# Kernel tuning notes

Hardware: AMD Instinct MI355X
Metric: run time of the kernel (lower is better)

## Reference

```python
import jax, jax.numpy as jnp
import numpy as np

B, C, H, W = 16, 256, 64, 64
E = 8           # num_experts
TOPK = 2
HID = int(C * 2.0)  # hidden_mult = 2.0 -> 512


def setup_inputs() -> dict:
    key = jax.random.key(0)
    ks = jax.random.split(key, 6)
    x = jax.random.normal(ks[0], (B, C, H, W), dtype=jnp.float32)
    Wr = jax.random.normal(ks[1], (C, E), dtype=jnp.float32) * 0.02
    br = jnp.zeros((E,), dtype=jnp.float32)
    W1 = jax.random.normal(ks[2], (E, C, HID), dtype=jnp.float32) * 0.02
    b1 = jnp.zeros((E, HID), dtype=jnp.float32)
    W2 = jax.random.normal(ks[3], (E, HID, C), dtype=jnp.float32) * 0.02
    b2 = jnp.zeros((E, C), dtype=jnp.float32)
    # nn.Parameter(torch.zeros(1)) in the original; use a small random value so
    scale = jax.random.normal(ks[4], (1,), dtype=jnp.float32) * 0.1
    return {"x": x, "Wr": Wr, "br": br, "W1": W1, "b1": b1,
            "W2": W2, "b2": b2, "scale": scale}


def reference(x, Wr, br, W1, b1, W2, b2, scale):
    b, c, h, w = x.shape
    tokens = jnp.transpose(x, (0, 2, 3, 1)).reshape(b, h * w, c)  # (B, T, C)
    logits = tokens @ Wr + br                                      # (B, T, E)
    topv, topi = jax.lax.top_k(logits, TOPK)                       # (B, T, K)
    wts = jax.nn.softmax(topv, axis=-1)                            # (B, T, K)

    out = jnp.zeros_like(tokens)
    num_experts = Wr.shape[1]
    for e in range(num_experts):
        # combine weight for expert e: sum of routing weights where selected
        we = jnp.sum(jnp.where(topi == e, wts, 0.0), axis=-1)      # (B, T)
        hdn = jax.nn.gelu(tokens @ W1[e] + b1[e], approximate=False)
        y = hdn @ W2[e] + b2[e]                                    # (B, T, C)
        out = out + y * we[..., None]

    out = jnp.transpose(out.reshape(b, h, w, c), (0, 3, 1, 2))     # (B, C, H, W)
    return x + scale[0] * out
```

## Files before the change

### kernel.cpp

```cpp
#include <hip/hip_runtime.h>
#include <hip/hip_bf16.h>
#include <math.h>

#define HW   4096
#define CCH  256
#define NE   8
#define HID  512
#define NTOK 65536
#define PADH 260

typedef short s16x8 __attribute__((ext_vector_type(8)));
typedef float f32x4 __attribute__((ext_vector_type(4)));
typedef unsigned short u16x8 __attribute__((ext_vector_type(8)));
typedef unsigned short u16x4 __attribute__((ext_vector_type(4)));

__device__ __forceinline__ float fast_gelu(float v) {
    float v2 = v * v;
    float s  = v * fmaf(0.10294324f, v2, 2.3022079f);
    float e  = exp2f(-s);
    return v * __builtin_amdgcn_rcpf(1.0f + e);
}

__device__ __forceinline__ float bfbits2f(unsigned short h) {
    return __uint_as_float(((unsigned)h) << 16);
}

__device__ __forceinline__ short f2bf_bits(float f) {
    __hip_bfloat16 b = __float2bfloat16(f);
    return *reinterpret_cast<short*>(&b);
}

__device__ __forceinline__ unsigned short f2bf_ubits(float f) {
    __hip_bfloat16 b = __float2bfloat16(f);
    return *reinterpret_cast<unsigned short*>(&b);
}

__global__ __launch_bounds__(256) void k_transpose_both(
    const float* __restrict__ W1, const float* __restrict__ W2,
    __hip_bfloat16* __restrict__ w1t, __hip_bfloat16* __restrict__ w2t,
    int* __restrict__ meta)
{
    __shared__ float t[64][65];
    if (blockIdx.x == 0 && threadIdx.x < 16) meta[threadIdx.x] = 0;
    int bb = blockIdx.x;
    const float* in; __hip_bfloat16* out; int R, CC;
    if (bb < 256) { in = W1; out = w1t; R = 256; CC = 512; }
    else          { in = W2; out = w2t; R = 512; CC = 256; bb -= 256; }
    int tilesC = CC >> 6;
    int per = (R >> 6) * tilesC;
    int e = bb / per, tt = bb % per;
    int r0 = (tt / tilesC) << 6, c0 = (tt % tilesC) << 6;
    const float* ip = in + (size_t)e * R * CC;
    __hip_bfloat16* op = out + (size_t)e * R * CC;
    int lane = threadIdx.x & 63, g = threadIdx.x >> 6;
    for (int i = 0; i < 16; i++) {
        int r = i * 4 + g;
        t[r][lane] = ip[(size_t)(r0 + r) * CC + c0 + lane];
    }
    __syncthreads();
    for (int i = 0; i < 16; i++) {
        int r = i * 4 + g;
        op[(size_t)(c0 + r) * R + r0 + lane] = __float2bfloat16(t[lane][r]);
    }
}

__global__ __launch_bounds__(256) void k_router(
    const float* __restrict__ x, const float* __restrict__ Wr, const float* __restrict__ br,
    __hip_bfloat16* __restrict__ tokens, int* __restrict__ pair, float2* __restrict__ wts,
    int* __restrict__ meta )
{
    __shared__ float xt[CCH][33];
    __shared__ float wrp[2304];
    __shared__ float lg[32][NE];
    __shared__ int lc[NE];
    int tid = threadIdx.x;
    int n0 = blockIdx.x * 32;
    int b = n0 >> 12, p0 = n0 & 4095;
    const float* xb = x + (size_t)b * CCH * HW + p0;
    for (int i = tid; i < CCH * NE; i += 256) wrp[i] = Wr[i];
    if (tid < NE) lc[tid] = 0;
    __syncthreads();
    int j = tid & 31, cg = tid >> 5;
    float pacc[8];
#pragma unroll
    for (int e = 0; e < 8; e++) pacc[e] = 0.f;
    for (int i = 0; i < 32; i++) {
        int c = cg + 8 * i;
        float xv = xb[(size_t)c * HW + j];
        xt[c][j] = xv;
        const float4* wp = (const float4*)(wrp + c * 8);
        float4 wa = wp[0], wb2 = wp[1];
        pacc[0] = fmaf(xv, wa.x, pacc[0]);
        pacc[1] = fmaf(xv, wa.y, pacc[1]);
        pacc[2] = fmaf(xv, wa.z, pacc[2]);
        pacc[3] = fmaf(xv, wa.w, pacc[3]);
        pacc[4] = fmaf(xv, wb2.x, pacc[4]);
        pacc[5] = fmaf(xv, wb2.y, pacc[5]);
        pacc[6] = fmaf(xv, wb2.z, pacc[6]);
        pacc[7] = fmaf(xv, wb2.w, pacc[7]);
    }
    __syncthreads();
    float* plg = wrp;
#pragma unroll
    for (int e = 0; e < 8; e++) plg[(cg * 32 + j) * 9 + e] = pacc[e];
    __syncthreads();
    {
        int jj = tid & 31, e = tid >> 5;
        float s = br[e];
#pragma unroll
        for (int g = 0; g < 8; g++) s += plg[(g * 32 + jj) * 9 + e];
        lg[jj][e] = s;
    }
    __syncthreads();
    if (tid < 32) {
        float v0 = -1e30f, v1 = -1e30f; int i0 = 0, i1 = 0;
        for (int e = 0; e < NE; e++) {
            float l = lg[tid][e];
            if (l > v0)      { v1 = v0; i1 = i0; v0 = l; i0 = e; }
            else if (l > v1) { v1 = l; i1 = e; }
        }
        float e1 = expf(v1 - v0);
        float s = 1.0f + e1;
        wts[n0 + tid] = make_float2(1.0f / s, e1 / s);
        pair[n0 + tid] = i0 | (i1 << 8);
        atomicAdd(&lc[i0], 1);
        atomicAdd(&lc[i1], 1);
    }
    __syncthreads();
    if (tid < NE && lc[tid] > 0) atomicAdd(&meta[tid], lc[tid]);
#pragma unroll
    for (int i = 0; i < 4; i++) {
        int c0 = (cg + 8 * i) * 8;
        s16x8 v;
#pragma unroll
        for (int k = 0; k < 8; k++) v[k] = f2bf_bits(xt[c0 + k][j]);
        *(s16x8*)(tokens + (size_t)(n0 + j) * CCH + c0) = v;
    }
}

__global__ __launch_bounds__(256) void k_scatter(
    const int* __restrict__ pair, const float2* __restrict__ wts,
    int* __restrict__ meta, int* __restrict__ assign_tok, float* __restrict__ assign_w,
    int2* __restrict__ tok_slots)
{
    __shared__ int lcount[NE];
    __shared__ int lbase[NE];
    __shared__ int soff[NE];
    int tid = threadIdx.x;
    int n = blockIdx.x * 256 + tid;
    if (tid < NE) lcount[tid] = 0;
    __syncthreads();
    int pr = pair[n];
    int e0 = pr & 0xff, e1 = (pr >> 8) & 0xff;
    int p0 = atomicAdd(&lcount[e0], 1);
    int p1 = atomicAdd(&lcount[e1], 1);
    __syncthreads();
    if (tid == 0) {
        int off = 0, toff = 0;
        for (int ee = 0; ee < NE; ee++) {
            soff[ee] = off;
            int c = meta[ee];
            if (blockIdx.x == 0) { meta[16 + ee] = off; meta[25 + ee] = toff; }
            off += c;
            toff += (c + 63) >> 6;
        }
        if (blockIdx.x == 0) { meta[24] = off; meta[33] = toff; meta[34] = toff; }
    }
    if (tid < NE) lbase[tid] = atomicAdd(&meta[8 + tid], lcount[tid]);
    __syncthreads();
    float2 w = wts[n];
    int s0 = soff[e0] + lbase[e0] + p0;
    int s1 = soff[e1] + lbase[e1] + p1;
    assign_tok[s0] = n; assign_w[s0] = w.x;
    assign_tok[s1] = n; assign_w[s1] = w.y;
    tok_slots[n] = make_int2(s0, s1);
}

__global__ __launch_bounds__(512, 4) void k_expert(
    const __hip_bfloat16* __restrict__ tokens,
    const __hip_bfloat16* __restrict__ w1t,
    const __hip_bfloat16* __restrict__ w2t,
    const float* __restrict__ b1, const float* __restrict__ b2,
    const int* __restrict__ meta,
    const int* __restrict__ assign_tok, const float* __restrict__ assign_w,
    __hip_bfloat16* __restrict__ ybuf)
{
    __shared__ __align__(16) __hip_bfloat16 Af[64 * 256];
    __shared__ __align__(16) __hip_bfloat16 Hs[64 * PADH];
    __shared__ float wrow[64];
    __shared__ int trow[64];

    int total = meta[34];
    int swz = (int)blockIdx.x;
    int bid = (swz & 7) * 257 + (swz >> 3);
    if (bid >= total) return;
    int e = 0;
    while (e < 7 && bid >= meta[25 + e + 1]) e++;
    int tile = bid - meta[25 + e];
    int cnt = meta[e];
    int r0 = tile << 6;
    int abase = meta[16 + e] + r0;
    int nrows = cnt - r0; if (nrows > 64) nrows = 64;

    int tid = threadIdx.x;
    if (tid < 64) {
        if (tid < nrows) { trow[tid] = assign_tok[abase + tid]; wrow[tid] = assign_w[abase + tid]; }
        else             { trow[tid] = 0; wrow[tid] = 0.0f; }
    }
    __syncthreads();

    {
        uint4* dst = (uint4*)Af;
#pragma unroll
        for (int j = 0; j < 4; j++) {
            int row = j * 16 + (tid & 15);
            int chunk = (tid >> 4) & 31;
            dst[j * 512 + tid] = ((const uint4*)(tokens + (size_t)trow[row] * CCH))[chunk];
        }
    }

    int lane = tid & 63, wv = tid >> 6;
    int quad = lane >> 4, l15 = lane & 15;

    const __hip_bfloat16* w1e = w1t + (size_t)e * HID * CCH;
    const __hip_bfloat16* w2e = w2t + (size_t)e * CCH * HID;
    const float* b1e = b1 + e * HID;
    const float* b2e = b2 + e * CCH;

    const s16x8* apb = (const s16x8*)Af + quad * 16 + l15;

    auto G1Q = [&](int h, int off) {
        return (const s16x8*)(w1e + (size_t)(h * 256 + wv * 32 + off + l15) * CCH) + quad;
    };
    auto G2Q = [&](int h, int off) {
        return (const s16x8*)(w2e + (size_t)(wv * 32 + off + l15) * HID + h * 256) + quad;
    };

    f32x4 oacc[4][2];
#pragma unroll
    for (int i = 0; i < 4; i++)
#pragma unroll
        for (int j = 0; j < 2; j++) oacc[i][j] = (f32x4){0.f, 0.f, 0.f, 0.f};

    s16x8 bf0 = G1Q(0, 0)[0], bf1 = G1Q(0, 16)[0];
    float ob0 = b2e[wv * 32 + l15];
    float ob1 = b2e[wv * 32 + 16 + l15];

    __syncthreads();

#pragma unroll
    for (int h = 0; h < 2; h++) {
        const s16x8* bq0 = G1Q(h, 0);
        const s16x8* bq1 = G1Q(h, 16);

        f32x4 hacc[4][2];
#pragma unroll
        for (int i = 0; i < 4; i++)
#pragma unroll
            for (int j = 0; j < 2; j++) hacc[i][j] = (f32x4){0.f, 0.f, 0.f, 0.f};

#pragma unroll
        for (int kk = 0; kk < 8; kk++) {
            s16x8 bn0, bn1;
            if (kk < 7) { bn0 = bq0[(kk + 1) * 4]; bn1 = bq1[(kk + 1) * 4]; }
            s16x8 af[4];
#pragma unroll
            for (int mt = 0; mt < 4; mt++) af[mt] = apb[mt * 512 + kk * 4 * 16];
            __builtin_amdgcn_s_setprio(1);
#pragma unroll
            for (int mt = 0; mt < 4; mt++) {
                hacc[mt][0] = __builtin_amdgcn_mfma_f32_16x16x32_bf16(af[mt], bf0, hacc[mt][0], 0, 0, 0);
                hacc[mt][1] = __builtin_amdgcn_mfma_f32_16x16x32_bf16(af[mt], bf1, hacc[mt][1], 0, 0, 0);
            }
            __builtin_amdgcn_s_setprio(0);
            bf0 = bn0; bf1 = bn1;
        }

        const s16x8* b2q0 = G2Q(h, 0);
        const s16x8* b2q1 = G2Q(h, 16);
        s16x8 cf0 = b2q0[0], cf1 = b2q1[0];
        float biasA = b1e[h * 256 + wv * 32 + l15];
        float biasB = b1e[h * 256 + wv * 32 + 16 + l15];
        if (h == 0) { bf0 = G1Q(1, 0)[0]; bf1 = G1Q(1, 16)[0]; }

        if (h == 1) __syncthreads();

#pragma unroll
        for (int nt = 0; nt < 2; nt++) {
            int cl = wv * 32 + nt * 16 + l15;
            float bias = nt ? biasB : biasA;
#pragma unroll
            for (int mt = 0; mt < 4; mt++)
#pragma unroll
                for (int r = 0; r < 4; r++) {
                    int row = mt * 16 + quad * 4 + r;
                    float v = hacc[mt][nt][r] + bias;
                    Hs[row * PADH + cl] = __float2bfloat16(fast_gelu(v));
                }
        }
        __syncthreads();

#pragma unroll
        for (int kk = 0; kk < 8; kk++) {
            s16x8 cn0, cn1;
            if (kk < 7) { cn0 = b2q0[(kk + 1) * 4]; cn1 = b2q1[(kk + 1) * 4]; }
            s16x8 hf[4];
#pragma unroll
            for (int mt = 0; mt < 4; mt++)
                hf[mt] = *(const s16x8*)(Hs + (mt * 16 + l15) * PADH + kk * 32 + quad * 8);
            __builtin_amdgcn_s_setprio(1);
#pragma unroll
            for (int mt = 0; mt < 4; mt++) {
                oacc[mt][0] = __builtin_amdgcn_mfma_f32_16x16x32_bf16(hf[mt], cf0, oacc[mt][0], 0, 0, 0);
                oacc[mt][1] = __builtin_amdgcn_mfma_f32_16x16x32_bf16(hf[mt], cf1, oacc[mt][1], 0, 0, 0);
            }
            __builtin_amdgcn_s_setprio(0);
            cf0 = cn0; cf1 = cn1;
        }
    }

#pragma unroll
    for (int nt = 0; nt < 2; nt++) {
        int cc = wv * 32 + nt * 16 + l15;
        float bias = nt ? ob1 : ob0;
#pragma unroll
        for (int mt = 0; mt < 4; mt++) {
#pragma unroll
            for (int r = 0; r < 4; r++) {
                int row = mt * 16 + quad * 4 + r;
                if (row < nrows) {
                    float v = (oacc[mt][nt][r] + bias) * wrow[row];
                    ybuf[(size_t)(abase + row) * CCH + cc] = __float2bfloat16(v);
                }
            }
        }
    }
}

__global__ __launch_bounds__(256) void k_combine(
    const float* __restrict__ x, const __hip_bfloat16* __restrict__ ybuf,
    const int2* __restrict__ tok_slots, const float* __restrict__ scale,
    float* __restrict__ out)
{
    __shared__ __align__(16) unsigned short moe[CCH][36];
    __shared__ int2 slots[32];
    int tid = threadIdx.x;
    int n0 = blockIdx.x * 32;
    if (tid < 32) slots[tid] = tok_slots[n0 + tid];
    __syncthreads();
    {
        int r = tid & 31, g0 = tid >> 5;
#pragma unroll
        for (int it = 0; it < 2; it++) {
            int g = g0 + 8 * it;
            int2 s = slots[r];
            const u16x8* px = (const u16x8*)(ybuf + (size_t)s.x * CCH + 16 * g);
            const u16x8* py = (const u16x8*)(ybuf + (size_t)s.y * CCH + 16 * g);
            u16x8 ax0 = px[0], ax1 = px[1], ay0 = py[0], ay1 = py[1];
#pragma unroll
            for (int k = 0; k < 8; k++) {
                moe[16 * g + k][r]     = f2bf_ubits(bfbits2f(ax0[k]) + bfbits2f(ay0[k]));
                moe[16 * g + 8 + k][r] = f2bf_ubits(bfbits2f(ax1[k]) + bfbits2f(ay1[k]));
            }
        }
    }
    __syncthreads();
    float sc = scale[0];
    int b = n0 >> 12, p0 = n0 & 4095;
    const float* xb = x + (size_t)b * CCH * HW + p0;
    float* ob = out + (size_t)b * CCH * HW + p0;
    int j = tid & 7, cbase = tid >> 3;
#pragma unroll
    for (int i = 0; i < 8; i++) {
        int c = cbase + 32 * i;
        float4 xv = *(const float4*)(xb + (size_t)c * HW + 4 * j);
        u16x4 mv = *(const u16x4*)&moe[c][4 * j];
        float4 o;
        o.x = xv.x + sc * bfbits2f(mv[0]);
        o.y = xv.y + sc * bfbits2f(mv[1]);
        o.z = xv.z + sc * bfbits2f(mv[2]);
        o.w = xv.w + sc * bfbits2f(mv[3]);
        *(float4*)(ob + (size_t)c * HW + 4 * j) = o;
    }
}

extern "C" void kernel_launch(void* const* d_in, const int* in_sizes, int n_in,
                              void* d_out, int out_size, void* d_ws, size_t ws_size,
                              hipStream_t stream)
{
    const float* x     = (const float*)d_in[0];
    const float* Wr    = (const float*)d_in[1];
    const float* br    = (const float*)d_in[2];
    const float* W1    = (const float*)d_in[3];
    const float* b1    = (const float*)d_in[4];
    const float* W2    = (const float*)d_in[5];
    const float* b2    = (const float*)d_in[6];
    const float* scale = (const float*)d_in[7];
    float* out = (float*)d_out;

    char* ws = (char*)d_ws;
    __hip_bfloat16* tokens = (__hip_bfloat16*)(ws);
    __hip_bfloat16* w1t    = (__hip_bfloat16*)(ws + 33554432);
    __hip_bfloat16* w2t    = (__hip_bfloat16*)(ws + 35651584);
    __hip_bfloat16* ybuf   = (__hip_bfloat16*)(ws + 37748736);
    int*    assign_tok = (int*)   (ws + 104857600);
    float*  assign_w   = (float*) (ws + 105381888);
    int2*   tok_slots  = (int2*)  (ws + 105906176);
    int*    pair       = (int*)   (ws + 106430464);
    float2* wts        = (float2*)(ws + 106692608);
    int*    meta       = (int*)   (ws + 107216896);

    k_transpose_both<<<512, 256, 0, stream>>>(W1, W2, w1t, w2t, meta);
    k_router<<<2048, 256, 0, stream>>>(x, Wr, br, tokens, pair, wts, meta);
    k_scatter<<<256, 256, 0, stream>>>(pair, wts, meta, assign_tok, assign_w, tok_slots);
    k_expert<<<2056, 512, 0, stream>>>(tokens, w1t, w2t, b1, b2, meta,
                                       assign_tok, assign_w, ybuf);
    k_combine<<<2048, 256, 0, stream>>>(x, ybuf, tok_slots, scale, out);
}
```

Measured before the change: 340.6 us.

## Rewrite expert kernel as single-wave 16-token tiles with register-resident hidden activations

The expert FFN kernel moves from 512-thread blocks over 64-token tiles to single-wave blocks over 16-token tiles. The first GEMM is computed transposed (weights as A operand), and the W2 rows are pre-permuted so the GELU output in MFMA accumulator layout can feed the second GEMM directly from registers. This removes the shared-memory hidden buffer and its barriers. The cost is that each wave now streams the full W1 and W2 of its expert for only 16 tokens, which raises weight traffic about fourfold and relies on L2 to absorb it.

```diff
diff --git a/kernel.cpp b/kernel.cpp
--- a/kernel.cpp
+++ b/kernel.cpp
@@ -7,7 +7,6 @@
 #define NE   8
 #define HID  512
 #define NTOK 65536
-#define PADH 260
 
 typedef short s16x8 __attribute__((ext_vector_type(8)));
 typedef float f32x4 __attribute__((ext_vector_type(4)));
@@ -35,6 +34,10 @@
     return *reinterpret_cast<unsigned short*>(&b);
 }
 
+__device__ __forceinline__ int hperm(int h) {
+    return (h & ~31) | (((h & 15) >> 2) << 3) | (((h >> 4) & 1) << 2) | (h & 3);
+}
+
 __global__ __launch_bounds__(256) void k_transpose_both(
     const float* __restrict__ W1, const float* __restrict__ W2,
     __hip_bfloat16* __restrict__ w1t, __hip_bfloat16* __restrict__ w2t,
@@ -43,9 +46,10 @@
     __shared__ float t[64][65];
     if (blockIdx.x == 0 && threadIdx.x < 16) meta[threadIdx.x] = 0;
     int bb = blockIdx.x;
+    int isW2 = bb >= 256;
     const float* in; __hip_bfloat16* out; int R, CC;
-    if (bb < 256) { in = W1; out = w1t; R = 256; CC = 512; }
-    else          { in = W2; out = w2t; R = 512; CC = 256; bb -= 256; }
+    if (!isW2) { in = W1; out = w1t; R = 256; CC = 512; }
+    else       { in = W2; out = w2t; R = 512; CC = 256; bb -= 256; }
     int tilesC = CC >> 6;
     int per = (R >> 6) * tilesC;
     int e = bb / per, tt = bb % per;
@@ -60,7 +64,9 @@
     __syncthreads();
     for (int i = 0; i < 16; i++) {
         int r = i * 4 + g;
-        op[(size_t)(c0 + r) * R + r0 + lane] = __float2bfloat16(t[lane][r]);
+        int h = r0 + lane;
+        int hp = isW2 ? hperm(h) : h;
+        op[(size_t)(c0 + r) * R + hp] = __float2bfloat16(t[lane][r]);
     }
 }
 
@@ -162,7 +168,7 @@
             int c = meta[ee];
             if (blockIdx.x == 0) { meta[16 + ee] = off; meta[25 + ee] = toff; }
             off += c;
-            toff += (c + 63) >> 6;
+            toff += (c + 15) >> 4;
         }
         if (blockIdx.x == 0) { meta[24] = off; meta[33] = toff; meta[34] = toff; }
     }
@@ -176,7 +182,7 @@
     tok_slots[n] = make_int2(s0, s1);
 }
 
-__global__ __launch_bounds__(512, 4) void k_expert(
+__global__ __launch_bounds__(64, 4) void k_expert(
     const __hip_bfloat16* __restrict__ tokens,
     const __hip_bfloat16* __restrict__ w1t,
     const __hip_bfloat16* __restrict__ w2t,
@@ -185,153 +191,109 @@
     const int* __restrict__ assign_tok, const float* __restrict__ assign_w,
     __hip_bfloat16* __restrict__ ybuf)
 {
-    __shared__ __align__(16) __hip_bfloat16 Af[64 * 256];
-    __shared__ __align__(16) __hip_bfloat16 Hs[64 * PADH];
-    __shared__ float wrow[64];
-    __shared__ int trow[64];
+    __shared__ __align__(16) __hip_bfloat16 Af[16 * 256];
 
     int total = meta[34];
     int swz = (int)blockIdx.x;
-    int bid = (swz & 7) * 257 + (swz >> 3);
+    int bid = (swz & 7) * 1025 + (swz >> 3);
     if (bid >= total) return;
     int e = 0;
     while (e < 7 && bid >= meta[25 + e + 1]) e++;
     int tile = bid - meta[25 + e];
     int cnt = meta[e];
-    int r0 = tile << 6;
+    int r0 = tile << 4;
     int abase = meta[16 + e] + r0;
-    int nrows = cnt - r0; if (nrows > 64) nrows = 64;
-
-    int tid = threadIdx.x;
-    if (tid < 64) {
-        if (tid < nrows) { trow[tid] = assign_tok[abase + tid]; wrow[tid] = assign_w[abase + tid]; }
-        else             { trow[tid] = 0; wrow[tid] = 0.0f; }
-    }
-    __syncthreads();
+    int nrows = cnt - r0; if (nrows > 16) nrows = 16;
+
+    int lane = threadIdx.x;
+    int quad = lane >> 4, l15 = lane & 15;
+
+    int tok = assign_tok[abase + (l15 < nrows ? l15 : 0)];
 
     {
-        uint4* dst = (uint4*)Af;
-#pragma unroll
-        for (int j = 0; j < 4; j++) {
-            int row = j * 16 + (tid & 15);
-            int chunk = (tid >> 4) & 31;
-            dst[j * 512 + tid] = ((const uint4*)(tokens + (size_t)trow[row] * CCH))[chunk];
-        }
-    }
-
-    int lane = tid & 63, wv = tid >> 6;
-    int quad = lane >> 4, l15 = lane & 15;
+        const uint4* tsrc = (const uint4*)(tokens + (size_t)tok * CCH);
+        uint4* afu = (uint4*)Af;
+#pragma unroll
+        for (int i = 0; i < 8; i++)
+            afu[i * 64 + lane] = tsrc[i * 4 + quad];
+    }
 
     const __hip_bfloat16* w1e = w1t + (size_t)e * HID * CCH;
     const __hip_bfloat16* w2e = w2t + (size_t)e * CCH * HID;
     const float* b1e = b1 + e * HID;
+
+    f32x4 oacc[16];
+#pragma unroll
+    for (int o = 0; o < 16; o++) oacc[o] = (f32x4){0.f, 0.f, 0.f, 0.f};
+
+    s16x8 wf0 = *((const s16x8*)(w1e + (size_t)(l15) * CCH) + quad);
+    s16x8 wf1 = *((const s16x8*)(w1e + (size_t)(16 + l15) * CCH) + quad);
+
+    for (int ch = 0; ch < 16; ch++) {
+        const s16x8* a0 = (const s16x8*)(w1e + (size_t)(ch * 32      + l15) * CCH) + quad;
+        const s16x8* a1 = (const s16x8*)(w1e + (size_t)(ch * 32 + 16 + l15) * CCH) + quad;
+
+        float bv0[4], bv1[4];
+#pragma unroll
+        for (int r = 0; r < 4; r++) {
+            bv0[r] = b1e[ch * 32 + quad * 4 + r];
+            bv1[r] = b1e[ch * 32 + 16 + quad * 4 + r];
+        }
+
+        f32x4 h0 = (f32x4){0.f, 0.f, 0.f, 0.f};
+        f32x4 h1 = (f32x4){0.f, 0.f, 0.f, 0.f};
+#pragma unroll
+        for (int kk = 0; kk < 8; kk++) {
+            s16x8 wn0, wn1;
+            if (kk < 7) { wn0 = a0[(kk + 1) * 4]; wn1 = a1[(kk + 1) * 4]; }
+            s16x8 tf = ((const s16x8*)Af)[kk * 64 + lane];
+            __builtin_amdgcn_s_setprio(1);
+            h0 = __builtin_amdgcn_mfma_f32_16x16x32_bf16(wf0, tf, h0, 0, 0, 0);
+            h1 = __builtin_amdgcn_mfma_f32_16x16x32_bf16(wf1, tf, h1, 0, 0, 0);
+            __builtin_amdgcn_s_setprio(0);
+            if (kk < 7) { wf0 = wn0; wf1 = wn1; }
+        }
+        if (ch < 15) {
+            wf0 = *((const s16x8*)(w1e + (size_t)((ch + 1) * 32      + l15) * CCH) + quad);
+            wf1 = *((const s16x8*)(w1e + (size_t)((ch + 1) * 32 + 16 + l15) * CCH) + quad);
+        }
+
+        s16x8 a2;
+#pragma unroll
+        for (int r = 0; r < 4; r++) {
+            a2[r]     = f2bf_bits(fast_gelu(h0[r] + bv0[r]));
+            a2[4 + r] = f2bf_bits(fast_gelu(h1[r] + bv1[r]));
+        }
+
+        const __hip_bfloat16* w2b = w2e + (size_t)l15 * HID + ch * 32;
+        s16x8 cf = *((const s16x8*)w2b + quad);
+#pragma unroll
+        for (int o = 0; o < 16; o++) {
+            s16x8 cn;
+            if (o < 15) cn = *((const s16x8*)(w2b + (size_t)(o + 1) * (16 * HID)) + quad);
+            __builtin_amdgcn_s_setprio(1);
+            oacc[o] = __builtin_amdgcn_mfma_f32_16x16x32_bf16(a2, cf, oacc[o], 0, 0, 0);
+            __builtin_amdgcn_s_setprio(0);
+            cf = cn;
+        }
+    }
+
     const float* b2e = b2 + e * CCH;
-
-    const s16x8* apb = (const s16x8*)Af + quad * 16 + l15;
-
-    auto G1Q = [&](int h, int off) {
-        return (const s16x8*)(w1e + (size_t)(h * 256 + wv * 32 + off + l15) * CCH) + quad;
-    };
-    auto G2Q = [&](int h, int off) {
-        return (const s16x8*)(w2e + (size_t)(wv * 32 + off + l15) * HID + h * 256) + quad;
-    };
-
-    f32x4 oacc[4][2];
-#pragma unroll
-    for (int i = 0; i < 4; i++)
-#pragma unroll
-        for (int j = 0; j < 2; j++) oacc[i][j] = (f32x4){0.f, 0.f, 0.f, 0.f};
-
-    s16x8 bf0 = G1Q(0, 0)[0], bf1 = G1Q(0, 16)[0];
-    float ob0 = b2e[wv * 32 + l15];
-    float ob1 = b2e[wv * 32 + 16 + l15];
-
-    __syncthreads();
-
-#pragma unroll
-    for (int h = 0; h < 2; h++) {
-        const s16x8* bq0 = G1Q(h, 0);
-        const s16x8* bq1 = G1Q(h, 16);
-
-        f32x4 hacc[4][2];
-#pragma unroll
-        for (int i = 0; i < 4; i++)
-#pragma unroll
-            for (int j = 0; j < 2; j++) hacc[i][j] = (f32x4){0.f, 0.f, 0.f, 0.f};
-
-#pragma unroll
-        for (int kk = 0; kk < 8; kk++) {
-            s16x8 bn0, bn1;
-            if (kk < 7) { bn0 = bq0[(kk + 1) * 4]; bn1 = bq1[(kk + 1) * 4]; }
-            s16x8 af[4];
-#pragma unroll
-            for (int mt = 0; mt < 4; mt++) af[mt] = apb[mt * 512 + kk * 4 * 16];
-            __builtin_amdgcn_s_setprio(1);
-#pragma unroll
-            for (int mt = 0; mt < 4; mt++) {
-                hacc[mt][0] = __builtin_amdgcn_mfma_f32_16x16x32_bf16(af[mt], bf0, hacc[mt][0], 0, 0, 0);
-                hacc[mt][1] = __builtin_amdgcn_mfma_f32_16x16x32_bf16(af[mt], bf1, hacc[mt][1], 0, 0, 0);
-            }
-            __builtin_amdgcn_s_setprio(0);
-            bf0 = bn0; bf1 = bn1;
-        }
-
-        const s16x8* b2q0 = G2Q(h, 0);
-        const s16x8* b2q1 = G2Q(h, 16);
-        s16x8 cf0 = b2q0[0], cf1 = b2q1[0];
-        float biasA = b1e[h * 256 + wv * 32 + l15];
-        float biasB = b1e[h * 256 + wv * 32 + 16 + l15];
-        if (h == 0) { bf0 = G1Q(1, 0)[0]; bf1 = G1Q(1, 16)[0]; }
-
-        if (h == 1) __syncthreads();
-
-#pragma unroll
-        for (int nt = 0; nt < 2; nt++) {
-            int cl = wv * 32 + nt * 16 + l15;
-            float bias = nt ? biasB : biasA;
-#pragma unroll
-            for (int mt = 0; mt < 4; mt++)
-#pragma unroll
-                for (int r = 0; r < 4; r++) {
-                    int row = mt * 16 + quad * 4 + r;
-                    float v = hacc[mt][nt][r] + bias;
-                    Hs[row * PADH + cl] = __float2bfloat16(fast_gelu(v));
-                }
-        }
-        __syncthreads();
-
-#pragma unroll
-        for (int kk = 0; kk < 8; kk++) {
-            s16x8 cn0, cn1;
-            if (kk < 7) { cn0 = b2q0[(kk + 1) * 4]; cn1 = b2q1[(kk + 1) * 4]; }
-            s16x8 hf[4];
-#pragma unroll
-            for (int mt = 0; mt < 4; mt++)
-                hf[mt] = *(const s16x8*)(Hs + (mt * 16 + l15) * PADH + kk * 32 + quad * 8);
-            __builtin_amdgcn_s_setprio(1);
-#pragma unroll
-            for (int mt = 0; mt < 4; mt++) {
-                oacc[mt][0] = __builtin_amdgcn_mfma_f32_16x16x32_bf16(hf[mt], cf0, oacc[mt][0], 0, 0, 0);
-                oacc[mt][1] = __builtin_amdgcn_mfma_f32_16x16x32_bf16(hf[mt], cf1, oacc[mt][1], 0, 0, 0);
-            }
-            __builtin_amdgcn_s_setprio(0);
-            cf0 = cn0; cf1 = cn1;
-        }
-    }
-
-#pragma unroll
-    for (int nt = 0; nt < 2; nt++) {
-        int cc = wv * 32 + nt * 16 + l15;
-        float bias = nt ? ob1 : ob0;
-#pragma unroll
-        for (int mt = 0; mt < 4; mt++) {
-#pragma unroll
-            for (int r = 0; r < 4; r++) {
-                int row = mt * 16 + quad * 4 + r;
-                if (row < nrows) {
-                    float v = (oacc[mt][nt][r] + bias) * wrow[row];
-                    ybuf[(size_t)(abase + row) * CCH + cc] = __float2bfloat16(v);
-                }
+    float wr_[4];
+#pragma unroll
+    for (int r = 0; r < 4; r++) {
+        int row = quad * 4 + r;
+        wr_[r] = (row < nrows) ? assign_w[abase + row] : 0.0f;
+    }
+#pragma unroll
+    for (int o = 0; o < 16; o++) {
+        float bias = b2e[o * 16 + l15];
+#pragma unroll
+        for (int r = 0; r < 4; r++) {
+            int row = quad * 4 + r;
+            if (row < nrows) {
+                float v = (oacc[o][r] + bias) * wr_[r];
+                ybuf[(size_t)(abase + row) * CCH + o * 16 + l15] = __float2bfloat16(v);
             }
         }
     }
@@ -413,7 +375,7 @@
     k_transpose_both<<<512, 256, 0, stream>>>(W1, W2, w1t, w2t, meta);
     k_router<<<2048, 256, 0, stream>>>(x, Wr, br, tokens, pair, wts, meta);
     k_scatter<<<256, 256, 0, stream>>>(pair, wts, meta, assign_tok, assign_w, tok_slots);
-    k_expert<<<2056, 512, 0, stream>>>(tokens, w1t, w2t, b1, b2, meta,
-                                       assign_tok, assign_w, ybuf);
+    k_expert<<<8200, 64, 0, stream>>>(tokens, w1t, w2t, b1, b2, meta,
+                                      assign_tok, assign_w, ybuf);
     k_combine<<<2048, 256, 0, stream>>>(x, ybuf, tok_slots, scale, out);
 }
```

After: 793.4 us. 2.33x slower.
